# Performance work log

Hardware: AMD Instinct MI355X
Metric: run time of the kernel (lower is better)

Reference implementation:

```python
import jax, jax.numpy as jnp
import numpy as np

N_LAYERS = 3
N_NODES = 100000
N_EDGES = 1600000
D = 32


def setup_inputs() -> dict:
    key = jax.random.key(0)
    k1, k2, k3, k4 = jax.random.split(key, 4)
    edge_row = jax.random.randint(k1, (N_EDGES,), 0, N_NODES, dtype=jnp.int64 if jax.config.jax_enable_x64 else jnp.int32)
    edge_col = jax.random.randint(k2, (N_EDGES,), 0, N_NODES, dtype=edge_row.dtype)
    edge_val = jax.random.uniform(k3, (N_EDGES,), dtype=jnp.float32)
    x = jax.random.normal(k4, (N_NODES, D), dtype=jnp.float32)
    return {"edge_row": edge_row, "edge_col": edge_col, "edge_val": edge_val, "x": x}


def _spmm(edge_row, edge_col, edge_val, h):
    # y[r] = sum_{edges e with row r} val[e] * h[col[e]]  -- COO SpMM
    msgs = edge_val[:, None] * h[edge_col]  # [E, D]
    return jax.ops.segment_sum(msgs, edge_row, num_segments=N_NODES)


def reference(edge_row, edge_col, edge_val, x):
    # LightGCN propagation: mean over layer-0..n_layers embeddings
    out = x
    acc = x
    for _ in range(N_LAYERS):
        out = _spmm(edge_row, edge_col, edge_val, out)
        acc = acc + out
    return acc / jnp.asarray(N_LAYERS + 1, dtype=x.dtype)
```

## Files before the change

### kernel.cpp

```cpp
#include <hip/hip_runtime.h>
#include <hip/hip_fp16.h>


#define NN 100000
#define NE 1600000
#define DD 32
#define CHUNK 4096
#define NCHUNK ((NE + CHUNK - 1) / CHUNK)
#define BROWS 128
#define NBKT ((NN + BROWS - 1) / BROWS)
#define LDSE 3072

__device__ __forceinline__ unsigned f2bf(float f) {
    unsigned u = __float_as_uint(f);
    return (u + 0x7fffu + ((u >> 16) & 1u)) >> 16;
}

__device__ __forceinline__ unsigned f2h15(float v) {
    return (unsigned)__half_as_ushort(__float2half(v)) & 0x7fffu;
}
__device__ __forceinline__ float h152f(unsigned u) {
    return __half2float(__ushort_as_half((unsigned short)(u & 0x7fffu)));
}


__global__ __launch_bounds__(1024) void hist_kernel(
    const int* __restrict__ row, int* __restrict__ H)
{
    __shared__ int cnt[NBKT];
    const int tid = threadIdx.x;
    const int start = blockIdx.x * CHUNK;
    const int n = min(CHUNK, NE - start);
    for (int k = tid; k < NBKT; k += 1024) cnt[k] = 0;
    __syncthreads();
    const int j = tid * 4;
    if (j + 3 < n) {
        int4 r4 = *(const int4*)(row + start + j);
        atomicAdd(&cnt[r4.x >> 7], 1);
        atomicAdd(&cnt[r4.y >> 7], 1);
        atomicAdd(&cnt[r4.z >> 7], 1);
        atomicAdd(&cnt[r4.w >> 7], 1);
    } else {
        for (int k = j; k < n; k++) atomicAdd(&cnt[row[start + k] >> 7], 1);
    }
    __syncthreads();
    int* Hrow = H + (size_t)blockIdx.x * NBKT;
    for (int k = tid; k < NBKT; k += 1024) Hrow[k] = cnt[k];
}


__global__ __launch_bounds__(1024) void scan_tr_kernel(
    const int* __restrict__ H, int* __restrict__ Pt, int* __restrict__ tot)
{
    const int b = blockIdx.x * 16 + (threadIdx.x >> 6);
    if (b >= NBKT) return;
    const int lane = threadIdx.x & 63;
    int run = 0;
    #pragma unroll
    for (int c0 = 0; c0 < NCHUNK; c0 += 64) {
        int c = c0 + lane;
        int v = (c < NCHUNK) ? H[(size_t)c * NBKT + b] : 0;
        int x = v;
        #pragma unroll
        for (int off = 1; off < 64; off <<= 1) {
            int y = __shfl_up(x, off, 64);
            if (lane >= off) x += y;
        }
        if (c < NCHUNK) Pt[(size_t)b * NCHUNK + c] = run + x - v;
        run += __shfl(x, 63, 64);
    }
    if (lane == 0) tot[b] = run;
}


__global__ __launch_bounds__(1024) void scan_buckets_kernel(
    const int* __restrict__ tot, int* __restrict__ bucketbase,
    int* __restrict__ row_ptr)
{
    const int tid = threadIdx.x;
    int v = (tid < NBKT) ? tot[tid] : 0;
    int lane = tid & 63, w = tid >> 6;
    int x = v;
    #pragma unroll
    for (int off = 1; off < 64; off <<= 1) {
        int y = __shfl_up(x, off, 64);
        if (lane >= off) x += y;
    }
    __shared__ int wt[16];
    if (lane == 63) wt[w] = x;
    __syncthreads();
    if (w == 0 && lane < 16) {
        int y = wt[lane];
        #pragma unroll
        for (int off = 1; off < 16; off <<= 1) {
            int z = __shfl_up(y, off, 16);
            if ((lane & 15) >= off) y += z;
        }
        wt[lane] = y;
    }
    __syncthreads();
    int wo = (w > 0) ? wt[w - 1] : 0;
    int excl = x + wo - v;
    if (tid < NBKT) bucketbase[tid] = excl;
    if (tid == NBKT) { bucketbase[NBKT] = NE; row_ptr[NN] = NE; }
}


__global__ __launch_bounds__(1024) void scatter_kernel(
    const int* __restrict__ row, const int* __restrict__ col,
    const float* __restrict__ val, const int* __restrict__ bucketbase,
    const int* __restrict__ Pt, int2* __restrict__ tmp)
{
    __shared__ int cnt[NBKT];
    __shared__ int lbase[NBKT];
    __shared__ int gofs[NBKT];
    __shared__ int wt[16];
    __shared__ int2 recs[CHUNK];
    __shared__ int dest[CHUNK];
    const int tid = threadIdx.x;
    const int start = blockIdx.x * CHUNK;
    const int n = min(CHUNK, NE - start);
    for (int k = tid; k < NBKT; k += 1024) cnt[k] = 0;
    __syncthreads();

    int rrow[CHUNK / 1024], rcol[CHUNK / 1024], rank[CHUNK / 1024];
    float rval[CHUNK / 1024];
    #pragma unroll
    for (int k = 0; k < CHUNK / 1024; k++) {
        int j = k * 1024 + tid;
        if (j < n) {
            int r = row[start + j];
            rrow[k] = r;
            rcol[k] = col[start + j];
            rval[k] = val[start + j];
            rank[k] = atomicAdd(&cnt[r >> 7], 1);
        } else {
            rrow[k] = -1;
        }
    }
    __syncthreads();

    int v = (tid < NBKT) ? cnt[tid] : 0;
    {
        int lane = tid & 63, w = tid >> 6;
        int x = v;
        #pragma unroll
        for (int off = 1; off < 64; off <<= 1) {
            int y = __shfl_up(x, off, 64);
            if (lane >= off) x += y;
        }
        if (lane == 63) wt[w] = x;
        __syncthreads();
        if (w == 0 && lane < 16) {
            int y = wt[lane];
            #pragma unroll
            for (int off = 1; off < 16; off <<= 1) {
                int z = __shfl_up(y, off, 16);
                if ((lane & 15) >= off) y += z;
            }
            wt[lane] = y;
        }
        __syncthreads();
        int excl = x + ((w > 0) ? wt[w - 1] : 0) - v;
        if (tid < NBKT) {
            lbase[tid] = excl;
            gofs[tid] = bucketbase[tid] + Pt[(size_t)tid * NCHUNK + blockIdx.x];
        }
    }
    __syncthreads();

    #pragma unroll
    for (int k = 0; k < CHUNK / 1024; k++) {
        if (rrow[k] >= 0) {
            int b = rrow[k] >> 7;
            int p = lbase[b] + rank[k];
            recs[p] = make_int2(((rrow[k] & 127) << 17) | rcol[k],
                                __float_as_int(rval[k]));
            dest[p] = gofs[b] + rank[k];
        }
    }
    __syncthreads();

    for (int p = tid; p < n; p += 1024)
        tmp[dest[p]] = recs[p];
}


__global__ __launch_bounds__(512) void bucket_sort_kernel(
    const int* __restrict__ bucketbase, const int2* __restrict__ tmp,
    int* __restrict__ row_ptr, unsigned* __restrict__ edges,
    const float2* __restrict__ xin2, unsigned* __restrict__ hb0)
{
    __shared__ int cntw[8][BROWS];
    __shared__ int curw[8][BROWS];
    __shared__ int wt2[2];
    __shared__ unsigned ed[LDSE];
    const int tid = threadIdx.x;
    const int w   = tid >> 6;
    const int b   = blockIdx.x;
    const int s   = bucketbase[b];
    const int e   = bucketbase[b + 1];
    const int tot = e - s;

    #pragma unroll
    for (int k = 0; k < 4; k++) {
        int j = b * 2048 + k * 512 + tid;
        if (j < NN * 16) {
            float2 f = xin2[j];
            hb0[j] = f2bf(f.x) | (f2bf(f.y) << 16);
        }
    }

    for (int k = tid; k < 8 * BROWS; k += 512) (&cntw[0][0])[k] = 0;
    __syncthreads();

    int2 rc[6];
    #pragma unroll
    for (int k = 0; k < 6; k++) {
        int j = s + k * 512 + tid;
        rc[k] = (j < e && j < s + LDSE) ? tmp[j] : make_int2(-1, 0);
        if (rc[k].x >= 0) atomicAdd(&cntw[w][rc[k].x >> 17], 1);
    }
    if (tot > LDSE)
        for (int j = s + LDSE + tid; j < e; j += 512)
            atomicAdd(&cntw[w][tmp[j].x >> 17], 1);
    __syncthreads();

    int v = 0, x = 0;
    if (tid < BROWS) {
        int d = 0;
        #pragma unroll
        for (int ww = 0; ww < 8; ww++) d += cntw[ww][tid];
        v = d;
        int lane = tid & 63;
        x = v;
        #pragma unroll
        for (int off = 1; off < 64; off <<= 1) {
            int y = __shfl_up(x, off, 64);
            if (lane >= off) x += y;
        }
        if (lane == 63) wt2[tid >> 6] = x;
    }
    __syncthreads();
    if (tid < BROWS) {
        int excl = x + ((tid >> 6) ? wt2[0] : 0) - v;
        int r = b * BROWS + tid;
        if (r < NN) row_ptr[r] = s + excl;
        int run = excl;
        #pragma unroll
        for (int ww = 0; ww < 8; ww++) { curw[ww][tid] = run; run += cntw[ww][tid]; }
    }
    __syncthreads();

    if (tot <= LDSE) {
        #pragma unroll
        for (int k = 0; k < 6; k++) {
            if (rc[k].x >= 0) {
                int pos = atomicAdd(&curw[w][rc[k].x >> 17], 1);
                ed[pos] = ((unsigned)(rc[k].x & 0x1FFFF) << 15)
                        | f2h15(__int_as_float(rc[k].y));
            }
        }
        __syncthreads();
        for (int k = tid; k < tot; k += 512)
            edges[s + k] = ed[k];
    } else {
        #pragma unroll
        for (int k = 0; k < 6; k++) {
            if (rc[k].x >= 0) {
                int pos = atomicAdd(&curw[w][rc[k].x >> 17], 1);
                edges[s + pos] = ((unsigned)(rc[k].x & 0x1FFFF) << 15)
                               | f2h15(__int_as_float(rc[k].y));
            }
        }
        for (int j = s + LDSE + tid; j < e; j += 512) {
            int2 rec = tmp[j];
            int pos = atomicAdd(&curw[w][rec.x >> 17], 1);
            edges[s + pos] = ((unsigned)(rec.x & 0x1FFFF) << 15)
                           | f2h15(__int_as_float(rec.y));
        }
    }
}


template <int MODE>
__global__ __launch_bounds__(256) void spmm_kernel(
    const int* __restrict__ row_ptr, const unsigned* __restrict__ edges,
    const uint4* __restrict__ hb4,
    uint4* __restrict__ houtb4,
    const float4* __restrict__ xin4, float4* __restrict__ out4)
{
    const int g = blockIdx.x * 64 + (threadIdx.x >> 2);
    if (g >= NN) return;
    const int t = threadIdx.x & 3;
    const int s = row_ptr[g];
    const int e = row_ptr[g + 1];
    const int o = g * 8 + t * 2;

    float4 p0, p1;
    if (MODE == 0) { p0 = xin4[o]; p1 = xin4[o + 1]; }
    else           { p0 = out4[o]; p1 = out4[o + 1]; }

    float acc[8] = {0.f, 0.f, 0.f, 0.f, 0.f, 0.f, 0.f, 0.f};

#define ACC8(W, V)                                                         \
    do {                                                                   \
        acc[0] += (V) * __uint_as_float((W).x << 16);                      \
        acc[1] += (V) * __uint_as_float((W).x & 0xffff0000u);              \
        acc[2] += (V) * __uint_as_float((W).y << 16);                      \
        acc[3] += (V) * __uint_as_float((W).y & 0xffff0000u);              \
        acc[4] += (V) * __uint_as_float((W).z << 16);                      \
        acc[5] += (V) * __uint_as_float((W).z & 0xffff0000u);              \
        acc[6] += (V) * __uint_as_float((W).w << 16);                      \
        acc[7] += (V) * __uint_as_float((W).w & 0xffff0000u);              \
    } while (0)

    unsigned a0, a1, a2, a3, a4, a5, a6, a7;
    int i = s;
    if (i + 8 <= e) {
        a0 = edges[i];     a1 = edges[i + 1];
        a2 = edges[i + 2]; a3 = edges[i + 3];
        a4 = edges[i + 4]; a5 = edges[i + 5];
        a6 = edges[i + 6]; a7 = edges[i + 7];
    }
    for (; i + 16 <= e; i += 8) {
        uint4 w0 = hb4[(a0 >> 15) * 4 + t];
        uint4 w1 = hb4[(a1 >> 15) * 4 + t];
        uint4 w2 = hb4[(a2 >> 15) * 4 + t];
        uint4 w3 = hb4[(a3 >> 15) * 4 + t];
        uint4 w4 = hb4[(a4 >> 15) * 4 + t];
        uint4 w5 = hb4[(a5 >> 15) * 4 + t];
        uint4 w6 = hb4[(a6 >> 15) * 4 + t];
        uint4 w7 = hb4[(a7 >> 15) * 4 + t];
        unsigned b0 = edges[i + 8];  unsigned b1 = edges[i + 9];
        unsigned b2 = edges[i + 10]; unsigned b3 = edges[i + 11];
        unsigned b4 = edges[i + 12]; unsigned b5 = edges[i + 13];
        unsigned b6 = edges[i + 14]; unsigned b7 = edges[i + 15];
        ACC8(w0, h152f(a0)); ACC8(w1, h152f(a1));
        ACC8(w2, h152f(a2)); ACC8(w3, h152f(a3));
        ACC8(w4, h152f(a4)); ACC8(w5, h152f(a5));
        ACC8(w6, h152f(a6)); ACC8(w7, h152f(a7));
        a0 = b0; a1 = b1; a2 = b2; a3 = b3;
        a4 = b4; a5 = b5; a6 = b6; a7 = b7;
    }
    if (i + 8 <= e) {
        uint4 w0 = hb4[(a0 >> 15) * 4 + t];
        uint4 w1 = hb4[(a1 >> 15) * 4 + t];
        uint4 w2 = hb4[(a2 >> 15) * 4 + t];
        uint4 w3 = hb4[(a3 >> 15) * 4 + t];
        uint4 w4 = hb4[(a4 >> 15) * 4 + t];
        uint4 w5 = hb4[(a5 >> 15) * 4 + t];
        uint4 w6 = hb4[(a6 >> 15) * 4 + t];
        uint4 w7 = hb4[(a7 >> 15) * 4 + t];
        ACC8(w0, h152f(a0)); ACC8(w1, h152f(a1));
        ACC8(w2, h152f(a2)); ACC8(w3, h152f(a3));
        ACC8(w4, h152f(a4)); ACC8(w5, h152f(a5));
        ACC8(w6, h152f(a6)); ACC8(w7, h152f(a7));
        i += 8;
    }
    for (; i + 4 <= e; i += 4) {
        unsigned c0 = edges[i];
        unsigned c1 = edges[i + 1];
        unsigned c2 = edges[i + 2];
        unsigned c3 = edges[i + 3];
        uint4 w0 = hb4[(c0 >> 15) * 4 + t];
        uint4 w1 = hb4[(c1 >> 15) * 4 + t];
        uint4 w2 = hb4[(c2 >> 15) * 4 + t];
        uint4 w3 = hb4[(c3 >> 15) * 4 + t];
        ACC8(w0, h152f(c0)); ACC8(w1, h152f(c1));
        ACC8(w2, h152f(c2)); ACC8(w3, h152f(c3));
    }
    for (; i < e; ++i) {
        unsigned c0 = edges[i];
        uint4 w0 = hb4[(c0 >> 15) * 4 + t];
        ACC8(w0, h152f(c0));
    }
#undef ACC8

    if (MODE == 0 || MODE == 1) {
        uint4 p;
        p.x = f2bf(acc[0]) | (f2bf(acc[1]) << 16);
        p.y = f2bf(acc[2]) | (f2bf(acc[3]) << 16);
        p.z = f2bf(acc[4]) | (f2bf(acc[5]) << 16);
        p.w = f2bf(acc[6]) | (f2bf(acc[7]) << 16);
        houtb4[g * 4 + t] = p;
    }
    float4 lo, hi;
    if (MODE == 0 || MODE == 1) {
        lo = make_float4(p0.x + acc[0], p0.y + acc[1], p0.z + acc[2], p0.w + acc[3]);
        hi = make_float4(p1.x + acc[4], p1.y + acc[5], p1.z + acc[6], p1.w + acc[7]);
    } else {
        lo = make_float4((p0.x + acc[0]) * 0.25f, (p0.y + acc[1]) * 0.25f,
                         (p0.z + acc[2]) * 0.25f, (p0.w + acc[3]) * 0.25f);
        hi = make_float4((p1.x + acc[4]) * 0.25f, (p1.y + acc[5]) * 0.25f,
                         (p1.z + acc[6]) * 0.25f, (p1.w + acc[7]) * 0.25f);
    }
    out4[o] = lo;
    out4[o + 1] = hi;
}


extern "C" void kernel_launch(void* const* d_in, const int* in_sizes, int n_in,
                              void* d_out, int out_size, void* d_ws, size_t ws_size,
                              hipStream_t stream) {
    const int*   edge_row = (const int*)d_in[0];
    const int*   edge_col = (const int*)d_in[1];
    const float* edge_val = (const float*)d_in[2];
    const float* x        = (const float*)d_in[3];
    float* out = (float*)d_out;

    char* ws = (char*)d_ws;
    int*  H          = (int*)ws;   ws += (((size_t)NCHUNK * NBKT * 4) + 511) & ~511ull;
    int*  Pt         = (int*)ws;   ws += (((size_t)NBKT * NCHUNK * 4) + 511) & ~511ull;
    int*  tot        = (int*)ws;   ws += 4096;
    int*  bucketbase = (int*)ws;   ws += 4096;
    int*  row_ptr    = (int*)ws;   ws += ((size_t)(NN + 1) * 4 + 511) & ~511ull;
    int2* tmp        = (int2*)ws;  ws += (size_t)NE * 8 + 64;
    unsigned* edges  = (unsigned*)ws; ws += (size_t)NE * 4 + 64;
    unsigned* hb0    = (unsigned*)ws;  ws += (size_t)NN * DD * 2;
    unsigned* hb1    = (unsigned*)ws;  ws += (size_t)NN * DD * 2;

    hist_kernel        <<<NCHUNK, 1024, 0, stream>>>(edge_row, H);
    scan_tr_kernel     <<<(NBKT + 15) / 16, 1024, 0, stream>>>(H, Pt, tot);
    scan_buckets_kernel<<<1, 1024, 0, stream>>>(tot, bucketbase, row_ptr);
    scatter_kernel     <<<NCHUNK, 1024, 0, stream>>>(edge_row, edge_col, edge_val,
                                                     bucketbase, Pt, tmp);
    bucket_sort_kernel <<<NBKT, 512, 0, stream>>>(bucketbase, tmp, row_ptr, edges,
                                                  (const float2*)x, hb0);

    dim3 sp_grid((NN + 63) / 64);
    spmm_kernel<0><<<sp_grid, 256, 0, stream>>>(row_ptr, edges,
        (const uint4*)hb0, (uint4*)hb1, (const float4*)x, (float4*)out);
    spmm_kernel<1><<<sp_grid, 256, 0, stream>>>(row_ptr, edges,
        (const uint4*)hb1, (uint4*)hb0, (const float4*)x, (float4*)out);
    spmm_kernel<2><<<sp_grid, 256, 0, stream>>>(row_ptr, edges,
        (const uint4*)hb0, (uint4*)hb1, (const float4*)x, (float4*)out);
}
```

Measured before the change: 180.5 us.

## Defer layer accumulation to final SpMM and fuse bucket scan into scatter

The first two SpMM layers now only write bf16 embeddings; the final layer reads x plus the two stored bf16 layers and computes the mean, removing the fp32 output read/write from intermediate layers. The single-block bucket prefix scan is merged into the scatter kernel, with each block redundantly scanning totals, dropping one launch. This adds an extra bf16 buffer and uses bf16-rounded intermediate layers in the final sum.

```diff
diff --git a/kernel.cpp b/kernel.cpp
--- a/kernel.cpp
+++ b/kernel.cpp
@@ -22,6 +22,9 @@
 __device__ __forceinline__ float h152f(unsigned u) {
     return __half2float(__ushort_as_half((unsigned short)(u & 0x7fffu)));
 }
+
+#define BF_LO(u) __uint_as_float((u) << 16)
+#define BF_HI(u) __uint_as_float((u) & 0xffff0000u)
 
 
 __global__ __launch_bounds__(1024) void hist_kernel(
@@ -73,48 +76,16 @@
 }
 
 
-__global__ __launch_bounds__(1024) void scan_buckets_kernel(
-    const int* __restrict__ tot, int* __restrict__ bucketbase,
-    int* __restrict__ row_ptr)
-{
-    const int tid = threadIdx.x;
-    int v = (tid < NBKT) ? tot[tid] : 0;
-    int lane = tid & 63, w = tid >> 6;
-    int x = v;
-    #pragma unroll
-    for (int off = 1; off < 64; off <<= 1) {
-        int y = __shfl_up(x, off, 64);
-        if (lane >= off) x += y;
-    }
-    __shared__ int wt[16];
-    if (lane == 63) wt[w] = x;
-    __syncthreads();
-    if (w == 0 && lane < 16) {
-        int y = wt[lane];
-        #pragma unroll
-        for (int off = 1; off < 16; off <<= 1) {
-            int z = __shfl_up(y, off, 16);
-            if ((lane & 15) >= off) y += z;
-        }
-        wt[lane] = y;
-    }
-    __syncthreads();
-    int wo = (w > 0) ? wt[w - 1] : 0;
-    int excl = x + wo - v;
-    if (tid < NBKT) bucketbase[tid] = excl;
-    if (tid == NBKT) { bucketbase[NBKT] = NE; row_ptr[NN] = NE; }
-}
-
-
 __global__ __launch_bounds__(1024) void scatter_kernel(
     const int* __restrict__ row, const int* __restrict__ col,
-    const float* __restrict__ val, const int* __restrict__ bucketbase,
-    const int* __restrict__ Pt, int2* __restrict__ tmp)
+    const float* __restrict__ val, const int* __restrict__ tot,
+    const int* __restrict__ Pt, int2* __restrict__ tmp,
+    int* __restrict__ bucketbase_g)
 {
     __shared__ int cnt[NBKT];
     __shared__ int lbase[NBKT];
     __shared__ int gofs[NBKT];
-    __shared__ int wt[16];
+    __shared__ int wtA[16], wtB[16];
     __shared__ int2 recs[CHUNK];
     __shared__ int dest[CHUNK];
     const int tid = threadIdx.x;
@@ -140,32 +111,38 @@
     }
     __syncthreads();
 
-    int v = (tid < NBKT) ? cnt[tid] : 0;
+    int v1 = (tid < NBKT) ? cnt[tid] : 0;
+    int v2 = (tid < NBKT) ? tot[tid] : 0;
     {
         int lane = tid & 63, w = tid >> 6;
-        int x = v;
+        int x1 = v1, x2 = v2;
         #pragma unroll
         for (int off = 1; off < 64; off <<= 1) {
-            int y = __shfl_up(x, off, 64);
-            if (lane >= off) x += y;
-        }
-        if (lane == 63) wt[w] = x;
+            int y1 = __shfl_up(x1, off, 64);
+            int y2 = __shfl_up(x2, off, 64);
+            if (lane >= off) { x1 += y1; x2 += y2; }
+        }
+        if (lane == 63) { wtA[w] = x1; wtB[w] = x2; }
         __syncthreads();
         if (w == 0 && lane < 16) {
-            int y = wt[lane];
+            int y1 = wtA[lane], y2 = wtB[lane];
             #pragma unroll
             for (int off = 1; off < 16; off <<= 1) {
-                int z = __shfl_up(y, off, 16);
-                if ((lane & 15) >= off) y += z;
+                int z1 = __shfl_up(y1, off, 16);
+                int z2 = __shfl_up(y2, off, 16);
+                if ((lane & 15) >= off) { y1 += z1; y2 += z2; }
             }
-            wt[lane] = y;
+            wtA[lane] = y1; wtB[lane] = y2;
         }
         __syncthreads();
-        int excl = x + ((w > 0) ? wt[w - 1] : 0) - v;
+        int e1 = x1 + ((w > 0) ? wtA[w - 1] : 0) - v1;
+        int e2 = x2 + ((w > 0) ? wtB[w - 1] : 0) - v2;
         if (tid < NBKT) {
-            lbase[tid] = excl;
-            gofs[tid] = bucketbase[tid] + Pt[(size_t)tid * NCHUNK + blockIdx.x];
-        }
+            lbase[tid] = e1;
+            gofs[tid] = e2 + Pt[(size_t)tid * NCHUNK + blockIdx.x];
+            if (blockIdx.x == 0) bucketbase_g[tid] = e2;
+        }
+        if (blockIdx.x == 0 && tid == NBKT) bucketbase_g[NBKT] = NE;
     }
     __syncthreads();
 
@@ -245,7 +222,7 @@
     if (tid < BROWS) {
         int excl = x + ((tid >> 6) ? wt2[0] : 0) - v;
         int r = b * BROWS + tid;
-        if (r < NN) row_ptr[r] = s + excl;
+        if (r <= NN) row_ptr[r] = s + excl;
         int run = excl;
         #pragma unroll
         for (int ww = 0; ww < 8; ww++) { curw[ww][tid] = run; run += cntw[ww][tid]; }
@@ -283,11 +260,12 @@
 }
 
 
-template <int MODE>
+template <int FINAL>
 __global__ __launch_bounds__(256) void spmm_kernel(
     const int* __restrict__ row_ptr, const unsigned* __restrict__ edges,
     const uint4* __restrict__ hb4,
     uint4* __restrict__ houtb4,
+    const uint4* __restrict__ h1b4,
     const float4* __restrict__ xin4, float4* __restrict__ out4)
 {
     const int g = blockIdx.x * 64 + (threadIdx.x >> 2);
@@ -297,22 +275,25 @@
     const int e = row_ptr[g + 1];
     const int o = g * 8 + t * 2;
 
-    float4 p0, p1;
-    if (MODE == 0) { p0 = xin4[o]; p1 = xin4[o + 1]; }
-    else           { p0 = out4[o]; p1 = out4[o + 1]; }
+    float4 p0, p1; uint4 q1, q2;
+    if (FINAL) {
+        p0 = xin4[o]; p1 = xin4[o + 1];
+        q1 = h1b4[g * 4 + t];
+        q2 = hb4[g * 4 + t];
+    }
 
     float acc[8] = {0.f, 0.f, 0.f, 0.f, 0.f, 0.f, 0.f, 0.f};
 
 #define ACC8(W, V)                                                         \
     do {                                                                   \
-        acc[0] += (V) * __uint_as_float((W).x << 16);                      \
-        acc[1] += (V) * __uint_as_float((W).x & 0xffff0000u);              \
-        acc[2] += (V) * __uint_as_float((W).y << 16);                      \
-        acc[3] += (V) * __uint_as_float((W).y & 0xffff0000u);              \
-        acc[4] += (V) * __uint_as_float((W).z << 16);                      \
-        acc[5] += (V) * __uint_as_float((W).z & 0xffff0000u);              \
-        acc[6] += (V) * __uint_as_float((W).w << 16);                      \
-        acc[7] += (V) * __uint_as_float((W).w & 0xffff0000u);              \
+        acc[0] += (V) * BF_LO((W).x);                                      \
+        acc[1] += (V) * BF_HI((W).x);                                      \
+        acc[2] += (V) * BF_LO((W).y);                                      \
+        acc[3] += (V) * BF_HI((W).y);                                      \
+        acc[4] += (V) * BF_LO((W).z);                                      \
+        acc[5] += (V) * BF_HI((W).z);                                      \
+        acc[6] += (V) * BF_LO((W).w);                                      \
+        acc[7] += (V) * BF_HI((W).w);                                      \
     } while (0)
 
     unsigned a0, a1, a2, a3, a4, a5, a6, a7;
@@ -377,26 +358,26 @@
     }
 #undef ACC8
 
-    if (MODE == 0 || MODE == 1) {
+    if (!FINAL) {
         uint4 p;
         p.x = f2bf(acc[0]) | (f2bf(acc[1]) << 16);
         p.y = f2bf(acc[2]) | (f2bf(acc[3]) << 16);
         p.z = f2bf(acc[4]) | (f2bf(acc[5]) << 16);
         p.w = f2bf(acc[6]) | (f2bf(acc[7]) << 16);
         houtb4[g * 4 + t] = p;
-    }
-    float4 lo, hi;
-    if (MODE == 0 || MODE == 1) {
-        lo = make_float4(p0.x + acc[0], p0.y + acc[1], p0.z + acc[2], p0.w + acc[3]);
-        hi = make_float4(p1.x + acc[4], p1.y + acc[5], p1.z + acc[6], p1.w + acc[7]);
     } else {
-        lo = make_float4((p0.x + acc[0]) * 0.25f, (p0.y + acc[1]) * 0.25f,
-                         (p0.z + acc[2]) * 0.25f, (p0.w + acc[3]) * 0.25f);
-        hi = make_float4((p1.x + acc[4]) * 0.25f, (p1.y + acc[5]) * 0.25f,
-                         (p1.z + acc[6]) * 0.25f, (p1.w + acc[7]) * 0.25f);
-    }
-    out4[o] = lo;
-    out4[o + 1] = hi;
+        float4 lo, hi;
+        lo.x = (p0.x + BF_LO(q1.x) + BF_LO(q2.x) + acc[0]) * 0.25f;
+        lo.y = (p0.y + BF_HI(q1.x) + BF_HI(q2.x) + acc[1]) * 0.25f;
+        lo.z = (p0.z + BF_LO(q1.y) + BF_LO(q2.y) + acc[2]) * 0.25f;
+        lo.w = (p0.w + BF_HI(q1.y) + BF_HI(q2.y) + acc[3]) * 0.25f;
+        hi.x = (p1.x + BF_LO(q1.z) + BF_LO(q2.z) + acc[4]) * 0.25f;
+        hi.y = (p1.y + BF_HI(q1.z) + BF_HI(q2.z) + acc[5]) * 0.25f;
+        hi.z = (p1.z + BF_LO(q1.w) + BF_LO(q2.w) + acc[6]) * 0.25f;
+        hi.w = (p1.w + BF_HI(q1.w) + BF_HI(q2.w) + acc[7]) * 0.25f;
+        out4[o] = lo;
+        out4[o + 1] = hi;
+    }
 }
 
 
@@ -419,20 +400,21 @@
     unsigned* edges  = (unsigned*)ws; ws += (size_t)NE * 4 + 64;
     unsigned* hb0    = (unsigned*)ws;  ws += (size_t)NN * DD * 2;
     unsigned* hb1    = (unsigned*)ws;  ws += (size_t)NN * DD * 2;
-
-    hist_kernel        <<<NCHUNK, 1024, 0, stream>>>(edge_row, H);
-    scan_tr_kernel     <<<(NBKT + 15) / 16, 1024, 0, stream>>>(H, Pt, tot);
-    scan_buckets_kernel<<<1, 1024, 0, stream>>>(tot, bucketbase, row_ptr);
-    scatter_kernel     <<<NCHUNK, 1024, 0, stream>>>(edge_row, edge_col, edge_val,
-                                                     bucketbase, Pt, tmp);
-    bucket_sort_kernel <<<NBKT, 512, 0, stream>>>(bucketbase, tmp, row_ptr, edges,
-                                                  (const float2*)x, hb0);
+    unsigned* hb2    = (unsigned*)ws;  ws += (size_t)NN * DD * 2;
+
+    hist_kernel       <<<NCHUNK, 1024, 0, stream>>>(edge_row, H);
+    scan_tr_kernel    <<<(NBKT + 15) / 16, 1024, 0, stream>>>(H, Pt, tot);
+    scatter_kernel    <<<NCHUNK, 1024, 0, stream>>>(edge_row, edge_col, edge_val,
+                                                    tot, Pt, tmp, bucketbase);
+    bucket_sort_kernel<<<NBKT, 512, 0, stream>>>(bucketbase, tmp, row_ptr, edges,
+                                                 (const float2*)x, hb0);
 
     dim3 sp_grid((NN + 63) / 64);
     spmm_kernel<0><<<sp_grid, 256, 0, stream>>>(row_ptr, edges,
-        (const uint4*)hb0, (uint4*)hb1, (const float4*)x, (float4*)out);
+        (const uint4*)hb0, (uint4*)hb1, nullptr, nullptr, nullptr);
+    spmm_kernel<0><<<sp_grid, 256, 0, stream>>>(row_ptr, edges,
+        (const uint4*)hb1, (uint4*)hb2, nullptr, nullptr, nullptr);
     spmm_kernel<1><<<sp_grid, 256, 0, stream>>>(row_ptr, edges,
-        (const uint4*)hb1, (uint4*)hb0, (const float4*)x, (float4*)out);
-    spmm_kernel<2><<<sp_grid, 256, 0, stream>>>(row_ptr, edges,
-        (const uint4*)hb0, (uint4*)hb1, (const float4*)x, (float4*)out);
-}
+        (const uint4*)hb2, nullptr, (const uint4*)hb1,
+        (const float4*)x, (float4*)out);
+}
```

Result: faster. 174.3 us (-3.5%).
